# Kernel tuning notes

Measured on AMD Instinct MI355X. Metric: run time of the kernel, lower is better.

Reference implementation:

```python
import jax, jax.numpy as jnp
import numpy as np

KERNEL_SIZES = [1, 2, 3]
KERNEL_NUM = 11
SIGMA = 0.1
EXACT_SIGMA = 0.001
EMBED_DIM = 300
HIDDEN = 128
Q_VOCAB = 30000
D_VOCAB = 30000


def _mus_sigmas():
    mus, sigmas = [], []
    K = KERNEL_NUM
    for i in range(K):
        mu = 1.0 / (K - 1) + 2.0 * i / (K - 1) - 1.0
        sigma = SIGMA
        if mu > 1.0:
            sigma = EXACT_SIGMA
            mu = 1.0
        mus.append(mu)
        sigmas.append(sigma)
    return jnp.asarray(mus, jnp.float32), jnp.asarray(sigmas, jnp.float32)


def _conv_tanh(x_bcl, w, b, ks):
    # x_bcl: (B, C_in, L); ConstantPad1d((0, ks)) + Conv1d(kernel=ks+1) keeps length L
    y = jax.lax.conv_general_dilated(
        x_bcl, w, window_strides=(1,), padding=[(0, ks)],
        dimension_numbers=('NCW', 'OIW', 'NCW'))
    return jnp.tanh(y + b[None, :, None])  # (B, H, L)


def _l2norm(x):
    n = jnp.sqrt(jnp.sum(x * x, axis=-1, keepdims=True))
    return x / jnp.maximum(n, 1e-12)


def setup_inputs() -> dict:
    key = jax.random.key(0)
    ks = jax.random.split(key, 16)
    inp = {
        'query': jax.random.randint(ks[0], (128, 128), 0, Q_VOCAB),
        'doc': jax.random.randint(ks[1], (128, 512), 0, D_VOCAB),
        'q_emb': jax.random.normal(ks[2], (Q_VOCAB, EMBED_DIM), jnp.float32) * 0.1,
        'd_emb': jax.random.normal(ks[3], (D_VOCAB, EMBED_DIM), jnp.float32) * 0.1,
        'out_w': jax.random.normal(ks[4], (1, 3 * 3 * KERNEL_NUM), jnp.float32) * 0.1,
        'out_b': jnp.zeros((1,), jnp.float32),
    }
    for idx, k in enumerate(KERNEL_SIZES):
        fan_in = EMBED_DIM * (k + 1)
        inp[f'conv_w{idx}'] = jax.random.normal(ks[5 + 2 * idx], (HIDDEN, EMBED_DIM, k + 1), jnp.float32) / np.sqrt(fan_in)
        inp[f'conv_b{idx}'] = jnp.zeros((HIDDEN,), jnp.float32)
    return inp


def reference(query, doc, q_emb, d_emb, conv_w0, conv_b0, conv_w1, conv_b1,
              conv_w2, conv_b2, out_w, out_b):
    mus, sigmas = _mus_sigmas()
    inv2s2 = 1.0 / (2.0 * sigmas * sigmas)  # (K,)

    q_e = q_emb[query].transpose(0, 2, 1)  # (B, D, Lq)
    d_e = d_emb[doc].transpose(0, 2, 1)    # (B, D, Ld)

    cws = [(conv_w0, conv_b0), (conv_w1, conv_b1), (conv_w2, conv_b2)]
    # q_convs/d_convs share weights (same nn.Sequential appended to both lists)
    q_convs = [_l2norm(_conv_tanh(q_e, w, b, ks).transpose(0, 2, 1))
               for (w, b), ks in zip(cws, KERNEL_SIZES)]  # each (B, Lq, H)
    d_convs = [_l2norm(_conv_tanh(d_e, w, b, ks).transpose(0, 2, 1))
               for (w, b), ks in zip(cws, KERNEL_SIZES)]  # each (B, Ld, H)

    KM = []
    for qi in range(3):
        for di in range(3):
            mm = jnp.einsum('bld,brd->blr', q_convs[qi], d_convs[di])  # (B,Lq,Ld)
            # Gaussian kernel soft-histogram, vectorized over all kernels
            kern = jnp.exp(-(mm[..., None] - mus) ** 2 * inv2s2)  # (B,Lq,Ld,K)
            K = jnp.log1p(kern.sum(axis=2)).sum(axis=1)           # (B,K)
            KM.append(K)
    phi = jnp.concatenate(KM, axis=1)  # (B, 9*KERNEL_NUM)
    return phi @ out_w.T + out_b       # (B, 1)
```

## Files before the change

### kernel.cpp

```cpp
#include <hip/hip_runtime.h>
#include <hip/hip_bf16.h>

typedef __hip_bfloat16 bf16;
typedef __attribute__((ext_vector_type(8))) short short8;
typedef __attribute__((ext_vector_type(4))) float f32x4;
typedef __attribute__((ext_vector_type(2))) float f32x2;

#define NB 128
#define NH 128
#define NLQ 128
#define NLD 512
#define NEMB 300
#define XQROWS 132
#define XDROWS 516
#define XCOLS 320

__device__ __forceinline__ unsigned short bfbits(float x) {
    __hip_bfloat16 h = __float2bfloat16(x);
    return *reinterpret_cast<unsigned short*>(&h);
}

__device__ __forceinline__ float fast_tanh(float x) {
    x = fminf(9.f, fmaxf(-9.f, x));
    float e = __builtin_amdgcn_exp2f(x * 2.8853900817779268f);
    return (e - 1.f) * __builtin_amdgcn_rcpf(e + 1.f);
}

__global__ __launch_bounds__(256)
void pack_all(const int* __restrict__ q_tok, const int* __restrict__ d_tok,
              const float* __restrict__ q_emb, const float* __restrict__ d_emb,
              const float* __restrict__ cw0, const float* __restrict__ cw1,
              const float* __restrict__ cw2,
              bf16* __restrict__ Wp, bf16* __restrict__ Xq, bf16* __restrict__ Xd)
{
    int bx = blockIdx.x;
    if (bx < 1440) {
        int e = bx * 256 + threadIdx.x;
        int widx = (e >= 204800) ? 2 : (e >= 81920 ? 1 : 0);
        int off = (widx == 0) ? 0 : (widx == 1 ? 81920 : 204800);
        int el = e - off;
        int W = widx + 2;
        int ch = el >> 12;
        int cc = ch / W;
        int t  = ch - cc * W;
        int h  = (el >> 5) & 127;
        int cp = el & 31;
        int c  = cc * 32 + cp;
        const float* cw = (widx == 0) ? cw0 : (widx == 1 ? cw1 : cw2);
        float v = (c < NEMB) ? cw[(h * NEMB + c) * W + t] : 0.f;
        Wp[e] = __float2bfloat16(v);
        return;
    }
    int gid = (bx - 1440) * 256 + threadIdx.x;
    int row = gid / 20, g = gid - row * 20;
    const float* emb; bf16* dst; int tok;
    if (row < NB * XQROWS) {
        int b = row / XQROWS, l = row - b * XQROWS;
        tok = (l < NLQ) ? q_tok[b * NLQ + l] : -1;
        emb = q_emb;
        dst = Xq + (size_t)row * XCOLS + g * 16;
    } else {
        int rowd = row - NB * XQROWS;
        int b = rowd / XDROWS, l = rowd - b * XDROWS;
        tok = (l < NLD) ? d_tok[b * NLD + l] : -1;
        emb = d_emb;
        dst = Xd + (size_t)rowd * XCOLS + g * 16;
    }
    int c0 = g * 16;
    float4 v[4];
    #pragma unroll
    for (int q = 0; q < 4; ++q) {
        int c = c0 + q * 4;
        v[q] = make_float4(0.f, 0.f, 0.f, 0.f);
        if (tok >= 0 && c < NEMB)
            v[q] = *reinterpret_cast<const float4*>(emb + (size_t)tok * NEMB + c);
    }
    short8 o0, o1;
    o0[0] = (short)bfbits(v[0].x); o0[1] = (short)bfbits(v[0].y);
    o0[2] = (short)bfbits(v[0].z); o0[3] = (short)bfbits(v[0].w);
    o0[4] = (short)bfbits(v[1].x); o0[5] = (short)bfbits(v[1].y);
    o0[6] = (short)bfbits(v[1].z); o0[7] = (short)bfbits(v[1].w);
    o1[0] = (short)bfbits(v[2].x); o1[1] = (short)bfbits(v[2].y);
    o1[2] = (short)bfbits(v[2].z); o1[3] = (short)bfbits(v[2].w);
    o1[4] = (short)bfbits(v[3].x); o1[5] = (short)bfbits(v[3].y);
    o1[6] = (short)bfbits(v[3].z); o1[7] = (short)bfbits(v[3].w);
    *reinterpret_cast<short8*>(dst) = o0;
    *reinterpret_cast<short8*>(dst + 8) = o1;
}

__global__ __launch_bounds__(512, 4)
void conv_kernel(const bf16* __restrict__ Xq, const bf16* __restrict__ Xd,
                 const bf16* __restrict__ Wp,
                 const float* __restrict__ cb0, const float* __restrict__ cb1,
                 const float* __restrict__ cb2,
                 bf16* __restrict__ qn, bf16* __restrict__ dn)
{
    __shared__ bf16 Xs[2][2][132][40];
    __shared__ bf16 Bs[2][128][36];
    __shared__ float ssq[2][256];

    int bx = blockIdx.x;
    int widx = bx % 3;
    int inner = bx / 3;
    int W = widx + 2;
    const bf16* wp = Wp + ((widx == 0) ? 0 : (widx == 1 ? 81920 : 204800));
    const float* cb = (widx == 0) ? cb0 : (widx == 1 ? cb1 : cb2);

    int tid = threadIdx.x;
    int lane = tid & 63;
    int wv = tid >> 6;
    int wr = wv >> 1;
    int wc = wv & 1;
    int s_wave = wr >> 1;
    int lr_base = (wr & 1) * 64;

    bf16* outp; int L;
    int sb0, sb1, sl00, sl01;
    const bf16* xbase;
    size_t grow0, grow1;
    if (inner < 64) {
        outp = qn + (size_t)widx * NB * NLQ * NH;
        L = NLQ; sb0 = inner * 2; sb1 = sb0 + 1; sl00 = 0; sl01 = 0;
        xbase = Xq; grow0 = (size_t)sb0 * XQROWS; grow1 = (size_t)sb1 * XQROWS;
    } else {
        int i = inner - 64;
        outp = dn + (size_t)widx * NB * NLD * NH;
        L = NLD; sb0 = i >> 1; sb1 = sb0; sl00 = (i & 1) * 256; sl01 = sl00 + 128;
        xbase = Xd; grow0 = (size_t)sb0 * XDROWS + sl00; grow1 = grow0 + 128;
    }

    int sr = tid >> 2;
    int colg = tid & 3;
    const bf16* gsrc0 = xbase + (grow0 + sr) * XCOLS + colg * 8;
    const bf16* gsrc1 = xbase + (grow1 + sr) * XCOLS + colg * 8;
    bool has_tail = (tid >= 448 && tid < 480);
    int j = tid - 448;
    int ts = (j >> 2) >> 2, trr = 128 + ((j >> 2) & 3), tcolg = j & 3;
    const bf16* gsrcT = xbase + ((ts ? grow1 : grow0) + trr) * XCOLS + tcolg * 8;

    const short8* wp8 = reinterpret_cast<const short8*>(wp);
    int bh = tid >> 2, bcg = tid & 3;

    {
        short8 a0 = *reinterpret_cast<const short8*>(gsrc0);
        short8 a1 = *reinterpret_cast<const short8*>(gsrc1);
        short8 at;
        if (has_tail) at = *reinterpret_cast<const short8*>(gsrcT);
        short8 b0 = wp8[tid];
        *reinterpret_cast<short8*>(&Xs[0][0][sr][colg * 8]) = a0;
        *reinterpret_cast<short8*>(&Xs[0][1][sr][colg * 8]) = a1;
        if (has_tail) *reinterpret_cast<short8*>(&Xs[0][ts][trr][tcolg * 8]) = at;
        *reinterpret_cast<short8*>(&Bs[0][bh][bcg * 8]) = b0;
    }
    __syncthreads();

    f32x4 acc[4][4];
    #pragma unroll
    for (int m = 0; m < 4; ++m)
        #pragma unroll
        for (int n = 0; n < 4; ++n)
            acc[m][n] = (f32x4){0.f, 0.f, 0.f, 0.f};

    int nsteps = W * 10;
    int xcur = 0, bcur = 0, step = 0;
    short8 a0, a1, at;
    for (int cc = 0; cc < 10; ++cc) {
        if (cc < 9) {
            a0 = *reinterpret_cast<const short8*>(gsrc0 + (cc + 1) * 32);
            a1 = *reinterpret_cast<const short8*>(gsrc1 + (cc + 1) * 32);
            if (has_tail) at = *reinterpret_cast<const short8*>(gsrcT + (cc + 1) * 32);
        }
        for (int t = 0; t < W; ++t, ++step) {
            short8 nb;
            bool hn = (step + 1 < nsteps);
            if (hn) nb = wp8[(size_t)(step + 1) * 512 + tid];

            short8 bv[4], af[4];
            #pragma unroll
            for (int n = 0; n < 4; ++n)
                bv[n] = *reinterpret_cast<const short8*>(
                    &Bs[bcur][wc * 64 + n * 16 + (lane & 15)][(lane >> 4) * 8]);
            #pragma unroll
            for (int m = 0; m < 4; ++m)
                af[m] = *reinterpret_cast<const short8*>(
                    &Xs[xcur][s_wave][lr_base + m * 16 + (lane & 15) + t][(lane >> 4) * 8]);
            #pragma unroll
            for (int m = 0; m < 4; ++m)
                #pragma unroll
                for (int n = 0; n < 4; ++n)
                    acc[m][n] = __builtin_amdgcn_mfma_f32_16x16x32_bf16(af[m], bv[n], acc[m][n], 0, 0, 0);

            if (hn)
                *reinterpret_cast<short8*>(&Bs[bcur ^ 1][bh][bcg * 8]) = nb;
            if (t == W - 1 && cc < 9) {
                *reinterpret_cast<short8*>(&Xs[xcur ^ 1][0][sr][colg * 8]) = a0;
                *reinterpret_cast<short8*>(&Xs[xcur ^ 1][1][sr][colg * 8]) = a1;
                if (has_tail) *reinterpret_cast<short8*>(&Xs[xcur ^ 1][ts][trr][tcolg * 8]) = at;
            }
            if (hn || (t == W - 1 && cc < 9)) __syncthreads();
            bcur ^= 1;
            if (t == W - 1) xcur ^= 1;
        }
    }

    float ssl[4][4];
    #pragma unroll
    for (int m = 0; m < 4; ++m)
        #pragma unroll
        for (int i = 0; i < 4; ++i) ssl[m][i] = 0.f;

    #pragma unroll
    for (int n = 0; n < 4; ++n) {
        float bias = cb[wc * 64 + n * 16 + (lane & 15)];
        #pragma unroll
        for (int m = 0; m < 4; ++m)
            #pragma unroll
            for (int i = 0; i < 4; ++i) {
                float v = fast_tanh(acc[m][n][i] + bias);
                acc[m][n][i] = v;
                ssl[m][i] += v * v;
            }
    }
    #pragma unroll
    for (int m = 0; m < 4; ++m)
        #pragma unroll
        for (int i = 0; i < 4; ++i) {
            float s = ssl[m][i];
            s += __shfl_xor(s, 1); s += __shfl_xor(s, 2);
            s += __shfl_xor(s, 4); s += __shfl_xor(s, 8);
            ssl[m][i] = s;
        }
    if ((lane & 15) == 0) {
        #pragma unroll
        for (int m = 0; m < 4; ++m)
            #pragma unroll
            for (int i = 0; i < 4; ++i)
                ssq[wc][wr * 64 + m * 16 + (lane >> 4) * 4 + i] = ssl[m][i];
    }
    __syncthreads();
    #pragma unroll
    for (int m = 0; m < 4; ++m)
        #pragma unroll
        for (int i = 0; i < 4; ++i) {
            int r = wr * 64 + m * 16 + (lane >> 4) * 4 + i;
            float s2 = ssq[0][r] + ssq[1][r];
            float sc = 1.f / fmaxf(sqrtf(s2), 1e-12f);
            int s = r >> 7, lr = r & 127;
            int b = s ? sb1 : sb0;
            int l = (s ? sl01 : sl00) + lr;
            bf16* dst = outp + ((size_t)(b * L + l)) * NH;
            #pragma unroll
            for (int n = 0; n < 4; ++n)
                dst[wc * 64 + n * 16 + (lane & 15)] = __float2bfloat16(acc[m][n][i] * sc);
        }
}

__global__ __launch_bounds__(512, 4)
void sim_kernel(const bf16* __restrict__ qn, const bf16* __restrict__ dn,
                float* __restrict__ phi)
{
    __shared__ bf16 Qs[128][136];
    __shared__ bf16 Ds[64][136];
    __shared__ float wsum[2][11];
    float (*red)[128][11] = reinterpret_cast<float(*)[128][11]>(&Ds[0][0]);

    int blk = blockIdx.x;
    int b = blk / 9;
    int pair = blk - b * 9;
    int qi = pair / 3, di = pair - qi * 3;

    int tid = threadIdx.x, lane = tid & 63, wv = tid >> 6;
    int wr = wv >> 2;
    int wc = wv & 3;

    const bf16* qbase = qn + ((size_t)qi * NB + b) * (NLQ * NH);
    const bf16* dbase = dn + ((size_t)di * NB + b) * (NLD * NH);

    {
        int r = tid >> 2, h0 = (tid & 3) * 32;
        #pragma unroll
        for (int v = 0; v < 4; ++v)
            *reinterpret_cast<short8*>(&Qs[r][h0 + v * 8]) =
                *reinterpret_cast<const short8*>(qbase + (size_t)r * NH + h0 + v * 8);
    }

    int dr = tid >> 3, dc = (tid & 7) * 16;
    {
        short8 st[2];
        #pragma unroll
        for (int v = 0; v < 2; ++v)
            st[v] = *reinterpret_cast<const short8*>(dbase + (size_t)dr * NH + dc + v * 8);
        #pragma unroll
        for (int v = 0; v < 2; ++v)
            *reinterpret_cast<short8*>(&Ds[dr][dc + v * 8]) = st[v];
    }
    __syncthreads();

    f32x2 sums2[2][11];
    #pragma unroll
    for (int n = 0; n < 2; ++n)
        #pragma unroll
        for (int k = 0; k < 11; ++k) sums2[n][k] = (f32x2){0.f, 0.f};

    const float C1 = 1.8315638888734179e-2f;
    const float C2 = 3.3546262790251185e-4f;
    const float C3 = 6.1442123533282098e-6f;
    const float C4 = 1.1253517471925912e-7f;

    for (int cc = 0; cc < 8; ++cc) {
        f32x4 acc[2][2];
        #pragma unroll
        for (int m = 0; m < 2; ++m)
            #pragma unroll
            for (int n = 0; n < 2; ++n)
                acc[m][n] = (f32x4){0.f, 0.f, 0.f, 0.f};

        #pragma unroll
        for (int kc = 0; kc < 4; ++kc) {
            short8 af[2], bq[2];
            #pragma unroll
            for (int m = 0; m < 2; ++m)
                af[m] = *reinterpret_cast<const short8*>(
                    &Ds[wr * 32 + m * 16 + (lane & 15)][kc * 32 + (lane >> 4) * 8]);
            #pragma unroll
            for (int n = 0; n < 2; ++n)
                bq[n] = *reinterpret_cast<const short8*>(
                    &Qs[wc * 32 + n * 16 + (lane & 15)][kc * 32 + (lane >> 4) * 8]);
            #pragma unroll
            for (int m = 0; m < 2; ++m)
                #pragma unroll
                for (int n = 0; n < 2; ++n)
                    acc[m][n] = __builtin_amdgcn_mfma_f32_16x16x32_bf16(af[m], bq[n], acc[m][n], 0, 0, 0);
        }
        __syncthreads();

        short8 st[2];
        if (cc < 7) {
            #pragma unroll
            for (int v = 0; v < 2; ++v)
                st[v] = *reinterpret_cast<const short8*>(
                    dbase + (size_t)((cc + 1) * 64 + dr) * NH + dc + v * 8);
        }

        #pragma unroll
        for (int n = 0; n < 2; ++n)
            #pragma unroll
            for (int i = 0; i < 4; ++i) {
                f32x2 x2;
                x2.x = acc[0][n][i];
                x2.y = acc[1][n][i];
                f32x2 ax = x2 * 28.853900817779268f;
                f32x2 R, Ri, E4;
                R.x = __builtin_amdgcn_exp2f(ax.x);
                R.y = __builtin_amdgcn_exp2f(ax.y);
                Ri.x = __builtin_amdgcn_rcpf(R.x);
                Ri.y = __builtin_amdgcn_rcpf(R.y);
                f32x2 d4 = x2 + 0.1f;
                f32x2 t = d4 * d4 * (-72.134752044448169f);
                E4.x = __builtin_amdgcn_exp2f(t.x);
                E4.y = __builtin_amdgcn_exp2f(t.y);
                sums2[n][4] += E4;
                f32x2 u = E4 * R;
                sums2[n][5] += u;
                u *= R; u *= C1; sums2[n][6] += u;
                u *= R; u *= C2; sums2[n][7] += u;
                u *= R; u *= C3; sums2[n][8] += u;
                u *= R; u *= C4; sums2[n][9] += u;
                f32x2 w = E4 * Ri; w *= C1; sums2[n][3] += w;
                w *= Ri; w *= C2; sums2[n][2] += w;
                w *= Ri; w *= C3; sums2[n][1] += w;
                w *= Ri; w *= C4; sums2[n][0] += w;
                if (__any(fmaxf(x2.x, x2.y) > 0.98f)) {
                    f32x2 d1 = x2 - 1.0f;
                    f32x2 t1 = d1 * d1 * (-721347.52044448f);
                    f32x2 e;
                    e.x = __builtin_amdgcn_exp2f(t1.x);
                    e.y = __builtin_amdgcn_exp2f(t1.y);
                    sums2[n][10] += e;
                }
            }

        if (cc < 7) {
            #pragma unroll
            for (int v = 0; v < 2; ++v)
                *reinterpret_cast<short8*>(&Ds[dr][dc + v * 8]) = st[v];
            __syncthreads();
        }
    }

    #pragma unroll
    for (int n = 0; n < 2; ++n)
        #pragma unroll
        for (int k = 0; k < 11; ++k) {
            float s = sums2[n][k].x + sums2[n][k].y;
            s += __shfl_xor(s, 16);
            s += __shfl_xor(s, 32);
            sums2[n][k].x = s;
        }
    if ((lane >> 4) == 0) {
        #pragma unroll
        for (int n = 0; n < 2; ++n)
            #pragma unroll
            for (int k = 0; k < 11; ++k)
                red[wr][wc * 32 + n * 16 + (lane & 15)][k] = sums2[n][k].x;
    }
    __syncthreads();
    if (tid < 128) {
        float lv[11];
        #pragma unroll
        for (int k = 0; k < 11; ++k)
            lv[k] = log1pf(red[0][tid][k] + red[1][tid][k]);
        #pragma unroll
        for (int k = 0; k < 11; ++k) {
            float s = lv[k];
            s += __shfl_xor(s, 1); s += __shfl_xor(s, 2); s += __shfl_xor(s, 4);
            s += __shfl_xor(s, 8); s += __shfl_xor(s, 16); s += __shfl_xor(s, 32);
            lv[k] = s;
        }
        if ((tid & 63) == 0) {
            #pragma unroll
            for (int k = 0; k < 11; ++k) wsum[tid >> 6][k] = lv[k];
        }
    }
    __syncthreads();
    if (tid < 11) phi[b * 99 + pair * 11 + tid] = wsum[0][tid] + wsum[1][tid];
}

__global__ void final_kernel(const float* __restrict__ phi, const float* __restrict__ ow,
                             const float* __restrict__ obias, float* __restrict__ out)
{
    int b = threadIdx.x;
    float s = obias[0];
    #pragma unroll
    for (int j = 0; j < 99; ++j) s += phi[b * 99 + j] * ow[j];
    out[b] = s;
}

extern "C" void kernel_launch(void* const* d_in, const int* in_sizes, int n_in,
                              void* d_out, int out_size, void* d_ws, size_t ws_size,
                              hipStream_t stream)
{
    const int*   query = (const int*)d_in[0];
    const int*   doc   = (const int*)d_in[1];
    const float* q_emb = (const float*)d_in[2];
    const float* d_emb = (const float*)d_in[3];
    const float* out_w = (const float*)d_in[4];
    const float* out_b = (const float*)d_in[5];
    const float* cw0 = (const float*)d_in[6];
    const float* cb0 = (const float*)d_in[7];
    const float* cw1 = (const float*)d_in[8];
    const float* cb1 = (const float*)d_in[9];
    const float* cw2 = (const float*)d_in[10];
    const float* cb2 = (const float*)d_in[11];

    const size_t QN = (size_t)NB * NLQ * NH;
    const size_t DN = (size_t)NB * NLD * NH;
    const size_t XQN = (size_t)NB * XQROWS * XCOLS;
    const size_t XDN = (size_t)NB * XDROWS * XCOLS;

    bf16* Wp = (bf16*)d_ws;
    bf16* Xq = Wp + 368640;
    bf16* Xd = Xq + XQN;
    bf16* qn = Xd + XDN;
    bf16* dn = qn + 3 * QN;
    float* phi = (float*)(dn + 3 * DN);

    pack_all<<<7920, 256, 0, stream>>>(query, doc, q_emb, d_emb, cw0, cw1, cw2, Wp, Xq, Xd);
    conv_kernel<<<960, 512, 0, stream>>>(Xq, Xd, Wp, cb0, cb1, cb2, qn, dn);
    sim_kernel<<<NB * 9, 512, 0, stream>>>(qn, dn, phi);
    final_kernel<<<1, 128, 0, stream>>>(phi, out_w, out_b, (float*)d_out);
}
```

Baseline: 209.4 us.

## Hold Q fragments in registers and double-buffer doc tiles in shared memory

Query MFMA fragments are loaded once from shared memory into registers before the main loop, which frees the Q tile's shared space so it can serve as a second doc buffer. The doc tile for the next chunk is fetched from global memory at the top of each iteration and written into the alternate buffer, leaving one barrier per iteration instead of two. This aims to hide global-load latency behind the MFMA and Gaussian-kernel work and to cut LDS reads of Q. The cost is 32 extra VGPRs per thread for the Q fragments, which may hurt occupancy under the 512x4 launch bound.

```diff
diff --git a/kernel.cpp b/kernel.cpp
--- a/kernel.cpp
+++ b/kernel.cpp
@@ -259,10 +259,10 @@
 void sim_kernel(const bf16* __restrict__ qn, const bf16* __restrict__ dn,
                 float* __restrict__ phi)
 {
-    __shared__ bf16 Qs[128][136];
-    __shared__ bf16 Ds[64][136];
+    __shared__ bf16 QDs[2][64][136];
     __shared__ float wsum[2][11];
-    float (*red)[128][11] = reinterpret_cast<float(*)[128][11]>(&Ds[0][0]);
+    bf16* flat = &QDs[0][0][0];
+    float (*red)[128][11] = reinterpret_cast<float(*)[128][11]>(flat);
 
     int blk = blockIdx.x;
     int b = blk / 9;
@@ -280,19 +280,26 @@
         int r = tid >> 2, h0 = (tid & 3) * 32;
         #pragma unroll
         for (int v = 0; v < 4; ++v)
-            *reinterpret_cast<short8*>(&Qs[r][h0 + v * 8]) =
+            *reinterpret_cast<short8*>(flat + r * 136 + h0 + v * 8) =
                 *reinterpret_cast<const short8*>(qbase + (size_t)r * NH + h0 + v * 8);
     }
+    __syncthreads();
+
+    short8 bq[2][4];
+    #pragma unroll
+    for (int n = 0; n < 2; ++n)
+        #pragma unroll
+        for (int kc = 0; kc < 4; ++kc)
+            bq[n][kc] = *reinterpret_cast<const short8*>(
+                flat + (wc * 32 + n * 16 + (lane & 15)) * 136 + kc * 32 + (lane >> 4) * 8);
+    __syncthreads();
 
     int dr = tid >> 3, dc = (tid & 7) * 16;
     {
-        short8 st[2];
-        #pragma unroll
-        for (int v = 0; v < 2; ++v)
-            st[v] = *reinterpret_cast<const short8*>(dbase + (size_t)dr * NH + dc + v * 8);
-        #pragma unroll
-        for (int v = 0; v < 2; ++v)
-            *reinterpret_cast<short8*>(&Ds[dr][dc + v * 8]) = st[v];
+        short8 st0 = *reinterpret_cast<const short8*>(dbase + (size_t)dr * NH + dc);
+        short8 st1 = *reinterpret_cast<const short8*>(dbase + (size_t)dr * NH + dc + 8);
+        *reinterpret_cast<short8*>(&QDs[0][dr][dc]) = st0;
+        *reinterpret_cast<short8*>(&QDs[0][dr][dc + 8]) = st1;
     }
     __syncthreads();
 
@@ -307,7 +314,14 @@
     const float C3 = 6.1442123533282098e-6f;
     const float C4 = 1.1253517471925912e-7f;
 
+    int cur = 0;
     for (int cc = 0; cc < 8; ++cc) {
+        short8 st0, st1;
+        if (cc < 7) {
+            st0 = *reinterpret_cast<const short8*>(dbase + (size_t)((cc + 1) * 64 + dr) * NH + dc);
+            st1 = *reinterpret_cast<const short8*>(dbase + (size_t)((cc + 1) * 64 + dr) * NH + dc + 8);
+        }
+
         f32x4 acc[2][2];
         #pragma unroll
         for (int m = 0; m < 2; ++m)
@@ -317,29 +331,21 @@
 
         #pragma unroll
         for (int kc = 0; kc < 4; ++kc) {
-            short8 af[2], bq[2];
+            short8 af[2];
             #pragma unroll
             for (int m = 0; m < 2; ++m)
                 af[m] = *reinterpret_cast<const short8*>(
-                    &Ds[wr * 32 + m * 16 + (lane & 15)][kc * 32 + (lane >> 4) * 8]);
-            #pragma unroll
-            for (int n = 0; n < 2; ++n)
-                bq[n] = *reinterpret_cast<const short8*>(
-                    &Qs[wc * 32 + n * 16 + (lane & 15)][kc * 32 + (lane >> 4) * 8]);
+                    &QDs[cur][wr * 32 + m * 16 + (lane & 15)][kc * 32 + (lane >> 4) * 8]);
             #pragma unroll
             for (int m = 0; m < 2; ++m)
                 #pragma unroll
                 for (int n = 0; n < 2; ++n)
-                    acc[m][n] = __builtin_amdgcn_mfma_f32_16x16x32_bf16(af[m], bq[n], acc[m][n], 0, 0, 0);
-        }
-        __syncthreads();
-
-        short8 st[2];
+                    acc[m][n] = __builtin_amdgcn_mfma_f32_16x16x32_bf16(af[m], bq[n][kc], acc[m][n], 0, 0, 0);
+        }
+
         if (cc < 7) {
-            #pragma unroll
-            for (int v = 0; v < 2; ++v)
-                st[v] = *reinterpret_cast<const short8*>(
-                    dbase + (size_t)((cc + 1) * 64 + dr) * NH + dc + v * 8);
+            *reinterpret_cast<short8*>(&QDs[cur ^ 1][dr][dc]) = st0;
+            *reinterpret_cast<short8*>(&QDs[cur ^ 1][dr][dc + 8]) = st1;
         }
 
         #pragma unroll
@@ -380,12 +386,8 @@
                 }
             }
 
-        if (cc < 7) {
-            #pragma unroll
-            for (int v = 0; v < 2; ++v)
-                *reinterpret_cast<short8*>(&Ds[dr][dc + v * 8]) = st[v];
-            __syncthreads();
-        }
+        __syncthreads();
+        cur ^= 1;
     }
 
     #pragma unroll
```

Result: no change. 208.3 us (-0.5%).
